# Performance work log

Hardware: AMD Instinct MI355X
Metric: run time of the kernel (lower is better)

The kernel has to match this reference:

```python
import jax, jax.numpy as jnp
import numpy as np

B, S, E = 4, 2048, 512
H, D = 8, 64  # n_head, attn_dim


def setup_inputs() -> dict:
    key = jax.random.key(0)
    ks = jax.random.split(key, 12)
    scale = 0.02
    return {
        "input_q": jax.random.normal(ks[0], (B, S, E), dtype=jnp.float32),
        "input_k": jax.random.normal(ks[1], (B, S, E), dtype=jnp.float32),
        "input_v": jax.random.normal(ks[2], (B, S, E), dtype=jnp.float32),
        "mask": jax.random.randint(ks[3], (B, S, S), 0, 2, dtype=jnp.int32),
        "wq": jax.random.normal(ks[4], (E, H * D), dtype=jnp.float32) * scale,
        "bq": jnp.zeros((H * D,), dtype=jnp.float32),
        "wk": jax.random.normal(ks[5], (E, H * D), dtype=jnp.float32) * scale,
        "bk": jnp.zeros((H * D,), dtype=jnp.float32),
        "wv": jax.random.normal(ks[6], (E, H * D), dtype=jnp.float32) * scale,
        "bv": jnp.zeros((H * D,), dtype=jnp.float32),
        "wo": jax.random.normal(ks[7], (H * D, E), dtype=jnp.float32) * scale,
        "bo": jnp.zeros((E,), dtype=jnp.float32),
    }


def reference(input_q, input_k, input_v, mask, wq, bq, wk, bk, wv, bv, wo, bo):
    b, lq, _ = input_q.shape
    lk = input_k.shape[1]
    # projections -> [b, len, H, D] -> [b, H, len, D]
    q = (input_q @ wq + bq).reshape(b, lq, H, D).transpose(0, 2, 1, 3)
    k = (input_k @ wk + bk).reshape(b, lk, H, D).transpose(0, 2, 1, 3)
    v = (input_v @ wv + bv).reshape(b, lk, H, D).transpose(0, 2, 1, 3)
    # raw scores [b, H, lq, lk]
    score = jnp.einsum("bhqd,bhkd->bhqk", q, k)
    # NOTE: original masks with -1e9 BEFORE dividing by sqrt(attn_dim)
    score = jnp.where(mask[:, None, :, :] == 0, jnp.float32(-1e9), score)
    attn = jax.nn.softmax(score / jnp.sqrt(jnp.float32(D)), axis=-1)
    out = jnp.einsum("bhqk,bhkd->bqhd", attn, v).reshape(b, lq, H * D)
    return out @ wo + bo
```

## Files before the change

### kernel.cpp

```cpp
#include <hip/hip_runtime.h>
#include <hip/hip_bf16.h>
#include <hip/hip_fp16.h>
#include <stdint.h>

#define Bc 4
#define Sc 2048
#define Ec 512
#define Hc 8
#define Dc 64
#define HDc 512

typedef __attribute__((ext_vector_type(8))) short bf16x8;
typedef __attribute__((ext_vector_type(4))) _Float16 f16x4;
typedef __attribute__((ext_vector_type(4))) float f32x4;
typedef unsigned int u32;

__device__ __forceinline__ unsigned short f2bf(float x) {
    union { float f; unsigned u; } v; v.f = x;
    unsigned r = v.u + 0x7FFFu + ((v.u >> 16) & 1u);
    return (unsigned short)(r >> 16);
}

__device__ __forceinline__ unsigned pkbf2(float a, float b) {
    float2 f; f.x = a; f.y = b;
    __hip_bfloat162 h = __float22bfloat162_rn(f);
    union { __hip_bfloat162 h2; unsigned u; } u; u.h2 = h;
    return u.u;
}

__device__ __forceinline__ unsigned short f2h(float x) {
    return __half_as_ushort(__float2half_rn(x));
}

__device__ __forceinline__ unsigned pkh2(float a, float b) {
    union { __half2 h2; unsigned u; } u;
    u.h2 = __floats2half2_rn(a, b);
    return u.u;
}

__device__ __forceinline__ uint4 pack8(float4 a, float4 b) {
    uint4 v;
    v.x = pkbf2(a.x, a.y); v.y = pkbf2(a.z, a.w);
    v.z = pkbf2(b.x, b.y); v.w = pkbf2(b.z, b.w);
    return v;
}

__device__ __forceinline__ void gload_lds(const void* g, void* l) {
    __builtin_amdgcn_global_load_lds(
        (const __attribute__((address_space(1))) u32*)g,
        (__attribute__((address_space(3))) u32*)l,
        16, 0, 0);
}

__global__ __launch_bounds__(256) void prep(
    const int* __restrict__ mask, unsigned long long* __restrict__ bits,
    const float* __restrict__ W0, const float* __restrict__ W1,
    const float* __restrict__ W2, const float* __restrict__ W3,
    unsigned short* __restrict__ Wt)
{
    const int blk = blockIdx.x;
    __shared__ float t[64][65];
    if (blk < 256) {
        const int z = blk >> 6;
        const float* W = z == 0 ? W0 : (z == 1 ? W1 : (z == 2 ? W2 : W3));
        unsigned short* O = Wt + (size_t)z * Ec * HDc;
        const int k0 = ((blk >> 3) & 7) * 64, n0 = (blk & 7) * 64;
#pragma unroll
        for (int i = 0; i < 16; i++) {
            int idx = threadIdx.x + 256 * i;
            int kr = idx >> 6, nc = idx & 63;
            t[nc][kr] = W[(size_t)(k0 + kr) * HDc + n0 + nc];
        }
        __syncthreads();
#pragma unroll
        for (int i = 0; i < 16; i++) {
            int idx = threadIdx.x + 256 * i;
            int nr = idx >> 6, kc = idx & 63;
            O[(size_t)(n0 + nr) * Ec + k0 + kc] = f2bf(t[nr][kc]);
        }
    } else {
        const int lane = threadIdx.x & 63;
        int wave = ((blk - 256) * 256 + (int)threadIdx.x) >> 6;
        const int nwaves = (2048 * 256) >> 6;
        const int nwords = (Bc * Sc * Sc) / 64;
        for (int w = wave; w < nwords; w += nwaves) {
            int m = mask[(size_t)w * 64 + lane];
            unsigned long long b = __ballot(m != 0);
            if (lane == 0) bits[w] = b;
        }
    }
}

__global__ __launch_bounds__(256) void proj_gemm(
    const float* __restrict__ Xq, const float* __restrict__ Xk, const float* __restrict__ Xv,
    const unsigned short* __restrict__ Wt,
    const float* __restrict__ bq, const float* __restrict__ bk, const float* __restrict__ bv,
    unsigned short* __restrict__ Oq, unsigned short* __restrict__ Ok,
    unsigned short* __restrict__ Vt)
{
    const int z = blockIdx.z;
    const float* X = z == 0 ? Xq : (z == 1 ? Xk : Xv);
    const unsigned short* Bt = Wt + (size_t)z * Ec * HDc;
    const float* bias = z == 0 ? bq : (z == 1 ? bk : bv);

    const int n0 = blockIdx.x * 128;
    const int m0 = blockIdx.y * 128;
    const int tid = threadIdx.x, lane = tid & 63, w = tid >> 6;
    const int c = lane & 15, quad = lane >> 4;
    const int wm = w & 1, wn = w >> 1;

    __shared__ unsigned short As[128 * 64];
    __shared__ unsigned short Bs[128 * 64];

    f32x4 acc[4][4];
#pragma unroll
    for (int i = 0; i < 4; i++)
#pragma unroll
        for (int j = 0; j < 4; j++) acc[i][j] = (f32x4){0.f, 0.f, 0.f, 0.f};

    for (int k0 = 0; k0 < Ec; k0 += 64) {
        __syncthreads();
#pragma unroll
        for (int jj = 0; jj < 4; jj++) {
            int rb = w * 32 + jj * 8;
            int row = rb + (lane >> 3);
            int dg = (lane & 7) ^ (row & 7);
            gload_lds(Bt + (size_t)(n0 + row) * Ec + k0 + dg * 8, &Bs[rb * 64]);
        }
#pragma unroll
        for (int s = 0; s < 4; s++) {
            int idx = tid + 256 * s;
            int row = idx >> 3, kp = idx & 7;
            int dg = kp ^ (row & 7);
            const float* src = X + (size_t)(m0 + row) * Ec + k0 + dg * 8;
            float4 fa = *(const float4*)src;
            float4 fb = *(const float4*)(src + 4);
            *(uint4*)&As[row * 64 + kp * 8] = pack8(fa, fb);
        }
        __syncthreads();
#pragma unroll
        for (int ks = 0; ks < 2; ks++) {
            int kg = ks * 4 + quad;
            bf16x8 af[4], bfr[4];
#pragma unroll
            for (int mt = 0; mt < 4; mt++) {
                int row = wm * 64 + mt * 16 + c;
                af[mt] = *(const bf16x8*)&As[row * 64 + ((kg ^ (row & 7)) * 8)];
            }
#pragma unroll
            for (int nt = 0; nt < 4; nt++) {
                int row = wn * 64 + nt * 16 + c;
                bfr[nt] = *(const bf16x8*)&Bs[row * 64 + ((kg ^ (row & 7)) * 8)];
            }
            if (z < 2) {
#pragma unroll
                for (int mt = 0; mt < 4; mt++)
#pragma unroll
                    for (int nt = 0; nt < 4; nt++)
                        acc[mt][nt] = __builtin_amdgcn_mfma_f32_16x16x32_bf16(af[mt], bfr[nt], acc[mt][nt], 0, 0, 0);
            } else {
#pragma unroll
                for (int mt = 0; mt < 4; mt++)
#pragma unroll
                    for (int nt = 0; nt < 4; nt++)
                        acc[mt][nt] = __builtin_amdgcn_mfma_f32_16x16x32_bf16(bfr[nt], af[mt], acc[mt][nt], 0, 0, 0);
            }
        }
    }

    if (z < 2) {
        unsigned short* O = z == 0 ? Oq : Ok;
        const float qs = z == 0 ? 0.125f : 1.0f;
#pragma unroll
        for (int mt = 0; mt < 4; mt++)
#pragma unroll
            for (int r = 0; r < 4; r++) {
                int gm = m0 + wm * 64 + mt * 16 + quad * 4 + r;
#pragma unroll
                for (int nt = 0; nt < 4; nt++) {
                    int gn = n0 + wn * 64 + nt * 16 + c;
                    O[(size_t)gm * HDc + gn] = f2bf((acc[mt][nt][r] + bias[gn]) * qs);
                }
            }
    } else {
#pragma unroll
        for (int mt = 0; mt < 4; mt++) {
            int gm = m0 + wm * 64 + mt * 16 + c;
            int bb = gm >> 11, sPos = gm & (Sc - 1);
#pragma unroll
            for (int nt = 0; nt < 4; nt++)
#pragma unroll
                for (int r = 0; r < 4; r++) {
                    int ng = n0 + wn * 64 + nt * 16 + quad * 4 + r;
                    int hh = ng >> 6, d = ng & 63;
                    Vt[((size_t)(bb * Hc + hh) * Dc + d) * Sc + sPos] = f2h(acc[mt][nt][r] + bias[ng]);
                }
        }
    }
}

__global__ __launch_bounds__(256, 4) void attn_kernel(
    const unsigned short* __restrict__ Qb, const unsigned short* __restrict__ Kb,
    const unsigned short* __restrict__ Vt, const unsigned long long* __restrict__ Mb,
    unsigned short* __restrict__ Ob)
{
    const int qt = blockIdx.x;
    const int h  = blockIdx.y;
    const int b  = blockIdx.z;
    const int q0 = qt * 64;
    const int tid = threadIdx.x, lane = tid & 63, w = tid >> 6;
    const int c = lane & 15, quad = lane >> 4;

    __shared__ unsigned short Ks[2][64 * 64];
    __shared__ unsigned short Vs[2][64 * 64];

    const int qg = q0 + w * 16 + c;
    const size_t qoff = ((size_t)b * Sc + qg) * HDc + h * Dc;

    bf16x8 qf[2];
    qf[0] = *(const bf16x8*)(Qb + qoff + quad * 8);
    qf[1] = *(const bf16x8*)(Qb + qoff + 32 + quad * 8);

    const unsigned long long* mr = Mb + ((size_t)b * Sc + qg) * (Sc / 64);
    const size_t kbase = ((size_t)b * Sc) * HDc + h * Dc;
    const size_t vbase = ((size_t)(b * Hc + h)) * Dc * Sc;

    f32x4 o[4], osum;
#pragma unroll
    for (int i = 0; i < 4; i++) o[i] = (f32x4){0.f, 0.f, 0.f, 0.f};
    osum = (f32x4){0.f, 0.f, 0.f, 0.f};

    const f16x4 ones = {(_Float16)1.0f, (_Float16)1.0f, (_Float16)1.0f, (_Float16)1.0f};

    auto stage = [&](int kt, int buf) {
#pragma unroll
        for (int j = 0; j < 2; j++) {
            int rb = w * 16 + j * 8;
            int row = rb + (lane >> 3);
            int dg = (lane & 7) ^ (row & 7);
            gload_lds(Kb + kbase + (size_t)(kt * 64 + row) * HDc + dg * 8, &Ks[buf][rb * 64]);
            gload_lds(Vt + vbase + (size_t)row * Sc + kt * 64 + dg * 8, &Vs[buf][rb * 64]);
        }
    };

    stage(0, 0);
    for (int kt = 0; kt < Sc / 64; kt++) {
        const int cur = kt & 1;
        unsigned long long mw = mr[kt];
        __syncthreads();
        if (kt + 1 < Sc / 64) stage(kt + 1, cur ^ 1);

        f32x4 s[4];
#pragma unroll
        for (int nt = 0; nt < 4; nt++) s[nt] = (f32x4){0.f, 0.f, 0.f, 0.f};
#pragma unroll
        for (int ks = 0; ks < 2; ks++) {
            int kg = ks * 4 + quad;
#pragma unroll
            for (int nt = 0; nt < 4; nt++) {
                int t = nt * 16 + c;
                bf16x8 a = *(const bf16x8*)&Ks[cur][t * 64 + ((kg ^ (t & 7)) * 8)];
                s[nt] = __builtin_amdgcn_mfma_f32_16x16x32_bf16(a, qf[ks], s[nt], 0, 0, 0);
            }
        }

        u32 mlo = (u32)(mw) >> (quad * 4);
        u32 mhi = (u32)(mw >> 32) >> (quad * 4);
        f16x4 pb[4];
#pragma unroll
        for (int nt = 0; nt < 4; nt++) {
            u32 msrc = (nt < 2) ? mlo : mhi;
            float p[4];
#pragma unroll
            for (int r = 0; r < 4; r++) {
                const int sh = (nt & 1) * 16 + r;
                int keep = ((int)(msrc << (31 - sh))) >> 31;
                float e = __expf(s[nt][r]);
                p[r] = __int_as_float(__float_as_int(e) & keep);
            }
            union { unsigned u[2]; f16x4 v; } pk;
            pk.u[0] = pkh2(p[0], p[1]);
            pk.u[1] = pkh2(p[2], p[3]);
            pb[nt] = pk.v;
        }

#pragma unroll
        for (int ntb = 0; ntb < 4; ntb++) {
#pragma unroll
            for (int dt = 0; dt < 4; dt++) {
                int d = dt * 16 + c;
                const f16x4 a = *(const f16x4*)&Vs[cur][d * 64 +
                    (((ntb * 2 + (quad >> 1)) ^ (d & 7)) * 8) + ((quad & 1) * 4)];
                o[dt] = __builtin_amdgcn_mfma_f32_16x16x16f16(a, pb[ntb], o[dt], 0, 0, 0);
            }
            osum = __builtin_amdgcn_mfma_f32_16x16x16f16(ones, pb[ntb], osum, 0, 0, 0);
        }
    }

    const float inv = 1.0f / osum[0];

#pragma unroll
    for (int nt = 0; nt < 4; nt++) {
        uint2 pk;
        pk.x = pkbf2(o[nt][0] * inv, o[nt][1] * inv);
        pk.y = pkbf2(o[nt][2] * inv, o[nt][3] * inv);
        *(uint2*)(Ob + qoff + nt * 16 + quad * 4) = pk;
    }
}

__global__ __launch_bounds__(256) void out_gemm(
    const unsigned short* __restrict__ Ab, const unsigned short* __restrict__ Bt,
    const float* __restrict__ bias, float* __restrict__ Out)
{
    const int n0 = blockIdx.x * 128;
    const int m0 = blockIdx.y * 64;
    const int tid = threadIdx.x, lane = tid & 63, w = tid >> 6;
    const int c = lane & 15, quad = lane >> 4;
    const int wm = w & 1, wn = w >> 1;

    __shared__ unsigned short As[64 * 64];
    __shared__ unsigned short Bs[128 * 64];

    f32x4 acc[2][4];
#pragma unroll
    for (int i = 0; i < 2; i++)
#pragma unroll
        for (int j = 0; j < 4; j++) acc[i][j] = (f32x4){0.f, 0.f, 0.f, 0.f};

    for (int k0 = 0; k0 < HDc; k0 += 64) {
        __syncthreads();
#pragma unroll
        for (int jj = 0; jj < 4; jj++) {
            int rb = w * 32 + jj * 8;
            int row = rb + (lane >> 3);
            int dg = (lane & 7) ^ (row & 7);
            gload_lds(Bt + (size_t)(n0 + row) * Ec + k0 + dg * 8, &Bs[rb * 64]);
        }
#pragma unroll
        for (int jj = 0; jj < 2; jj++) {
            int rb = w * 16 + jj * 8;
            int row = rb + (lane >> 3);
            int dg = (lane & 7) ^ (row & 7);
            gload_lds(Ab + (size_t)(m0 + row) * HDc + k0 + dg * 8, &As[rb * 64]);
        }
        __syncthreads();
#pragma unroll
        for (int ks = 0; ks < 2; ks++) {
            int kg = ks * 4 + quad;
            bf16x8 af[2], bfr[4];
#pragma unroll
            for (int mt = 0; mt < 2; mt++) {
                int row = wm * 32 + mt * 16 + c;
                af[mt] = *(const bf16x8*)&As[row * 64 + ((kg ^ (row & 7)) * 8)];
            }
#pragma unroll
            for (int nt = 0; nt < 4; nt++) {
                int row = wn * 64 + nt * 16 + c;
                bfr[nt] = *(const bf16x8*)&Bs[row * 64 + ((kg ^ (row & 7)) * 8)];
            }
#pragma unroll
            for (int mt = 0; mt < 2; mt++)
#pragma unroll
                for (int nt = 0; nt < 4; nt++)
                    acc[mt][nt] = __builtin_amdgcn_mfma_f32_16x16x32_bf16(af[mt], bfr[nt], acc[mt][nt], 0, 0, 0);
        }
    }
#pragma unroll
    for (int mt = 0; mt < 2; mt++)
#pragma unroll
        for (int r = 0; r < 4; r++) {
            int gm = m0 + wm * 32 + mt * 16 + quad * 4 + r;
#pragma unroll
            for (int nt = 0; nt < 4; nt++) {
                int gn = n0 + wn * 64 + nt * 16 + c;
                Out[(size_t)gm * Ec + gn] = acc[mt][nt][r] + bias[gn];
            }
        }
}

extern "C" void kernel_launch(void* const* d_in, const int* in_sizes, int n_in,
                              void* d_out, int out_size, void* d_ws, size_t ws_size,
                              hipStream_t stream)
{
    const float* xq = (const float*)d_in[0];
    const float* xk = (const float*)d_in[1];
    const float* xv = (const float*)d_in[2];
    const int* mask = (const int*)d_in[3];
    const float* wq = (const float*)d_in[4];
    const float* bq = (const float*)d_in[5];
    const float* wk = (const float*)d_in[6];
    const float* bk = (const float*)d_in[7];
    const float* wv = (const float*)d_in[8];
    const float* bv = (const float*)d_in[9];
    const float* wo = (const float*)d_in[10];
    const float* bo = (const float*)d_in[11];
    float* out = (float*)d_out;

    char* ws = (char*)d_ws;
    unsigned short* qb = (unsigned short*)(ws + (size_t)0 * 1024 * 1024);
    unsigned short* kb = (unsigned short*)(ws + (size_t)8 * 1024 * 1024);
    unsigned short* vt = (unsigned short*)(ws + (size_t)16 * 1024 * 1024);
    unsigned short* ab = (unsigned short*)(ws + (size_t)24 * 1024 * 1024);
    unsigned long long* mb = (unsigned long long*)(ws + (size_t)32 * 1024 * 1024);
    unsigned short* wt = (unsigned short*)(ws + (size_t)48 * 1024 * 1024);

    hipLaunchKernelGGL(prep, dim3(2304), dim3(256), 0, stream,
                       mask, mb, wq, wk, wv, wo, wt);

    const size_t WSZ = (size_t)Ec * HDc;
    hipLaunchKernelGGL(proj_gemm, dim3(4, 64, 3), dim3(256), 0, stream,
                       xq, xk, xv, wt, bq, bk, bv, qb, kb, vt);

    hipLaunchKernelGGL(attn_kernel, dim3(32, 8, 4), dim3(256), 0, stream,
                       qb, kb, vt, mb, ab);

    hipLaunchKernelGGL(out_gemm, dim3(4, 128), dim3(256), 0, stream,
                       ab, wt + 3 * WSZ, bo, out);
}
```

Baseline: 287.7 us.

## Pre-convert inputs to bf16, permute V layout, double query rows per attention wave

The prep kernel now also converts the fp32 Q/K/V inputs to bf16, so proj_gemm can stage A tiles with direct global-to-LDS loads instead of converting in registers. The V-transpose store uses a permuted sequence order so the attention kernel can read 8 fp16 values per LDS load. The attention kernel runs 128 threads per block with each wave handling 32 query rows, so every K/V fragment feeds two MFMA chains. The cost is a larger prep kernel with an extra bf16 round-trip through memory, plus more registers per wave in attention.

```diff
diff --git a/kernel.cpp b/kernel.cpp
--- a/kernel.cpp
+++ b/kernel.cpp
@@ -12,6 +12,7 @@
 
 typedef __attribute__((ext_vector_type(8))) short bf16x8;
 typedef __attribute__((ext_vector_type(4))) _Float16 f16x4;
+typedef __attribute__((ext_vector_type(8))) _Float16 f16x8;
 typedef __attribute__((ext_vector_type(4))) float f32x4;
 typedef unsigned int u32;
 
@@ -52,11 +53,17 @@
         16, 0, 0);
 }
 
+__device__ __forceinline__ int vperm(int mt, int c) {
+    return ((c >> 2) << 4) + ((mt >> 1) << 3) + ((mt & 1) << 2) + (c & 3);
+}
+
 __global__ __launch_bounds__(256) void prep(
     const int* __restrict__ mask, unsigned long long* __restrict__ bits,
     const float* __restrict__ W0, const float* __restrict__ W1,
     const float* __restrict__ W2, const float* __restrict__ W3,
-    unsigned short* __restrict__ Wt)
+    unsigned short* __restrict__ Wt,
+    const float* __restrict__ Xq, const float* __restrict__ Xk,
+    const float* __restrict__ Xv, unsigned short* __restrict__ Xb)
 {
     const int blk = blockIdx.x;
     __shared__ float t[64][65];
@@ -78,7 +85,7 @@
             int nr = idx >> 6, kc = idx & 63;
             O[(size_t)(n0 + nr) * Ec + k0 + kc] = f2bf(t[nr][kc]);
         }
-    } else {
+    } else if (blk < 2304) {
         const int lane = threadIdx.x & 63;
         int wave = ((blk - 256) * 256 + (int)threadIdx.x) >> 6;
         const int nwaves = (2048 * 256) >> 6;
@@ -88,18 +95,25 @@
             unsigned long long b = __ballot(m != 0);
             if (lane == 0) bits[w] = b;
         }
+    } else {
+        const int zi = blk - 2304;
+        const int z = zi >> 11, wi = zi & 2047;
+        const float* X = z == 0 ? Xq : (z == 1 ? Xk : Xv);
+        const size_t off = ((size_t)wi * 256 + threadIdx.x) * 8;
+        const float4* p = (const float4*)(X + off);
+        float4 f0 = p[0], f1 = p[1];
+        *(uint4*)(Xb + (size_t)z * 4194304 + off) = pack8(f0, f1);
     }
 }
 
 __global__ __launch_bounds__(256) void proj_gemm(
-    const float* __restrict__ Xq, const float* __restrict__ Xk, const float* __restrict__ Xv,
-    const unsigned short* __restrict__ Wt,
+    const unsigned short* __restrict__ Xb, const unsigned short* __restrict__ Wt,
     const float* __restrict__ bq, const float* __restrict__ bk, const float* __restrict__ bv,
     unsigned short* __restrict__ Oq, unsigned short* __restrict__ Ok,
     unsigned short* __restrict__ Vt)
 {
     const int z = blockIdx.z;
-    const float* X = z == 0 ? Xq : (z == 1 ? Xk : Xv);
+    const unsigned short* Xz = Xb + (size_t)z * 4194304;
     const unsigned short* Bt = Wt + (size_t)z * Ec * HDc;
     const float* bias = z == 0 ? bq : (z == 1 ? bk : bv);
 
@@ -126,16 +140,7 @@
             int row = rb + (lane >> 3);
             int dg = (lane & 7) ^ (row & 7);
             gload_lds(Bt + (size_t)(n0 + row) * Ec + k0 + dg * 8, &Bs[rb * 64]);
-        }
-#pragma unroll
-        for (int s = 0; s < 4; s++) {
-            int idx = tid + 256 * s;
-            int row = idx >> 3, kp = idx & 7;
-            int dg = kp ^ (row & 7);
-            const float* src = X + (size_t)(m0 + row) * Ec + k0 + dg * 8;
-            float4 fa = *(const float4*)src;
-            float4 fb = *(const float4*)(src + 4);
-            *(uint4*)&As[row * 64 + kp * 8] = pack8(fa, fb);
+            gload_lds(Xz + (size_t)(m0 + row) * Ec + k0 + dg * 8, &As[rb * 64]);
         }
         __syncthreads();
 #pragma unroll
@@ -187,19 +192,20 @@
         for (int mt = 0; mt < 4; mt++) {
             int gm = m0 + wm * 64 + mt * 16 + c;
             int bb = gm >> 11, sPos = gm & (Sc - 1);
+            int tbase = (sPos & ~63) + vperm(mt, c);
 #pragma unroll
             for (int nt = 0; nt < 4; nt++)
 #pragma unroll
                 for (int r = 0; r < 4; r++) {
                     int ng = n0 + wn * 64 + nt * 16 + quad * 4 + r;
                     int hh = ng >> 6, d = ng & 63;
-                    Vt[((size_t)(bb * Hc + hh) * Dc + d) * Sc + sPos] = f2h(acc[mt][nt][r] + bias[ng]);
+                    Vt[((size_t)(bb * Hc + hh) * Dc + d) * Sc + tbase] = f2h(acc[mt][nt][r] + bias[ng]);
                 }
         }
     }
 }
 
-__global__ __launch_bounds__(256, 4) void attn_kernel(
+__global__ __launch_bounds__(128, 2) void attn_kernel(
     const unsigned short* __restrict__ Qb, const unsigned short* __restrict__ Kb,
     const unsigned short* __restrict__ Vt, const unsigned long long* __restrict__ Mb,
     unsigned short* __restrict__ Ob)
@@ -214,28 +220,35 @@
     __shared__ unsigned short Ks[2][64 * 64];
     __shared__ unsigned short Vs[2][64 * 64];
 
-    const int qg = q0 + w * 16 + c;
-    const size_t qoff = ((size_t)b * Sc + qg) * HDc + h * Dc;
-
-    bf16x8 qf[2];
-    qf[0] = *(const bf16x8*)(Qb + qoff + quad * 8);
-    qf[1] = *(const bf16x8*)(Qb + qoff + 32 + quad * 8);
-
-    const unsigned long long* mr = Mb + ((size_t)b * Sc + qg) * (Sc / 64);
+    const int q_g0 = q0 + w * 32 + c;
+    const int q_g1 = q_g0 + 16;
+    const size_t qoff0 = ((size_t)b * Sc + q_g0) * HDc + h * Dc;
+    const size_t qoff1 = ((size_t)b * Sc + q_g1) * HDc + h * Dc;
+
+    bf16x8 qf0[2], qf1[2];
+#pragma unroll
+    for (int ks = 0; ks < 2; ks++) {
+        qf0[ks] = *(const bf16x8*)(Qb + qoff0 + ks * 32 + quad * 8);
+        qf1[ks] = *(const bf16x8*)(Qb + qoff1 + ks * 32 + quad * 8);
+    }
+
+    const unsigned long long* mr0 = Mb + ((size_t)b * Sc + q_g0) * (Sc / 64);
+    const unsigned long long* mr1 = Mb + ((size_t)b * Sc + q_g1) * (Sc / 64);
     const size_t kbase = ((size_t)b * Sc) * HDc + h * Dc;
     const size_t vbase = ((size_t)(b * Hc + h)) * Dc * Sc;
 
-    f32x4 o[4], osum;
-#pragma unroll
-    for (int i = 0; i < 4; i++) o[i] = (f32x4){0.f, 0.f, 0.f, 0.f};
-    osum = (f32x4){0.f, 0.f, 0.f, 0.f};
+    f32x4 o0[4], o1[4], osum0, osum1;
+#pragma unroll
+    for (int i = 0; i < 4; i++) { o0[i] = (f32x4){0.f,0.f,0.f,0.f}; o1[i] = (f32x4){0.f,0.f,0.f,0.f}; }
+    osum0 = (f32x4){0.f, 0.f, 0.f, 0.f};
+    osum1 = (f32x4){0.f, 0.f, 0.f, 0.f};
 
     const f16x4 ones = {(_Float16)1.0f, (_Float16)1.0f, (_Float16)1.0f, (_Float16)1.0f};
 
     auto stage = [&](int kt, int buf) {
 #pragma unroll
-        for (int j = 0; j < 2; j++) {
-            int rb = w * 16 + j * 8;
+        for (int j = 0; j < 4; j++) {
+            int rb = w * 32 + j * 8;
             int row = rb + (lane >> 3);
             int dg = (lane & 7) ^ (row & 7);
             gload_lds(Kb + kbase + (size_t)(kt * 64 + row) * HDc + dg * 8, &Ks[buf][rb * 64]);
@@ -246,13 +259,14 @@
     stage(0, 0);
     for (int kt = 0; kt < Sc / 64; kt++) {
         const int cur = kt & 1;
-        unsigned long long mw = mr[kt];
+        unsigned long long mw0 = mr0[kt];
+        unsigned long long mw1 = mr1[kt];
         __syncthreads();
         if (kt + 1 < Sc / 64) stage(kt + 1, cur ^ 1);
 
-        f32x4 s[4];
-#pragma unroll
-        for (int nt = 0; nt < 4; nt++) s[nt] = (f32x4){0.f, 0.f, 0.f, 0.f};
+        f32x4 s0[4], s1[4];
+#pragma unroll
+        for (int nt = 0; nt < 4; nt++) { s0[nt] = (f32x4){0.f,0.f,0.f,0.f}; s1[nt] = (f32x4){0.f,0.f,0.f,0.f}; }
 #pragma unroll
         for (int ks = 0; ks < 2; ks++) {
             int kg = ks * 4 + quad;
@@ -260,51 +274,65 @@
             for (int nt = 0; nt < 4; nt++) {
                 int t = nt * 16 + c;
                 bf16x8 a = *(const bf16x8*)&Ks[cur][t * 64 + ((kg ^ (t & 7)) * 8)];
-                s[nt] = __builtin_amdgcn_mfma_f32_16x16x32_bf16(a, qf[ks], s[nt], 0, 0, 0);
-            }
-        }
-
-        u32 mlo = (u32)(mw) >> (quad * 4);
-        u32 mhi = (u32)(mw >> 32) >> (quad * 4);
-        f16x4 pb[4];
+                s0[nt] = __builtin_amdgcn_mfma_f32_16x16x32_bf16(a, qf0[ks], s0[nt], 0, 0, 0);
+                s1[nt] = __builtin_amdgcn_mfma_f32_16x16x32_bf16(a, qf1[ks], s1[nt], 0, 0, 0);
+            }
+        }
+
+        u32 mlo0 = (u32)(mw0) >> (quad * 4), mhi0 = (u32)(mw0 >> 32) >> (quad * 4);
+        u32 mlo1 = (u32)(mw1) >> (quad * 4), mhi1 = (u32)(mw1 >> 32) >> (quad * 4);
+        f16x4 pb0[4], pb1[4];
 #pragma unroll
         for (int nt = 0; nt < 4; nt++) {
-            u32 msrc = (nt < 2) ? mlo : mhi;
-            float p[4];
+            u32 ms0 = (nt < 2) ? mlo0 : mhi0;
+            u32 ms1 = (nt < 2) ? mlo1 : mhi1;
+            float p0[4], p1[4];
 #pragma unroll
             for (int r = 0; r < 4; r++) {
                 const int sh = (nt & 1) * 16 + r;
-                int keep = ((int)(msrc << (31 - sh))) >> 31;
-                float e = __expf(s[nt][r]);
-                p[r] = __int_as_float(__float_as_int(e) & keep);
+                int k0 = ((int)(ms0 << (31 - sh))) >> 31;
+                int k1 = ((int)(ms1 << (31 - sh))) >> 31;
+                p0[r] = __int_as_float(__float_as_int(__expf(s0[nt][r])) & k0);
+                p1[r] = __int_as_float(__float_as_int(__expf(s1[nt][r])) & k1);
             }
             union { unsigned u[2]; f16x4 v; } pk;
-            pk.u[0] = pkh2(p[0], p[1]);
-            pk.u[1] = pkh2(p[2], p[3]);
-            pb[nt] = pk.v;
-        }
-
-#pragma unroll
-        for (int ntb = 0; ntb < 4; ntb++) {
+            pk.u[0] = pkh2(p0[0], p0[1]); pk.u[1] = pkh2(p0[2], p0[3]);
+            pb0[nt] = pk.v;
+            pk.u[0] = pkh2(p1[0], p1[1]); pk.u[1] = pkh2(p1[2], p1[3]);
+            pb1[nt] = pk.v;
+        }
+
+#pragma unroll
+        for (int a = 0; a < 2; a++) {
 #pragma unroll
             for (int dt = 0; dt < 4; dt++) {
                 int d = dt * 16 + c;
-                const f16x4 a = *(const f16x4*)&Vs[cur][d * 64 +
-                    (((ntb * 2 + (quad >> 1)) ^ (d & 7)) * 8) + ((quad & 1) * 4)];
-                o[dt] = __builtin_amdgcn_mfma_f32_16x16x16f16(a, pb[ntb], o[dt], 0, 0, 0);
-            }
-            osum = __builtin_amdgcn_mfma_f32_16x16x16f16(ones, pb[ntb], osum, 0, 0, 0);
-        }
-    }
-
-    const float inv = 1.0f / osum[0];
-
-#pragma unroll
-    for (int nt = 0; nt < 4; nt++) {
+                union { f16x8 v8; f16x4 v4[2]; } vv;
+                vv.v8 = *(const f16x8*)&Vs[cur][d * 64 + (((quad * 2 + a) ^ (d & 7)) * 8)];
+                o0[dt] = __builtin_amdgcn_mfma_f32_16x16x16f16(vv.v4[0], pb0[2*a],   o0[dt], 0, 0, 0);
+                o0[dt] = __builtin_amdgcn_mfma_f32_16x16x16f16(vv.v4[1], pb0[2*a+1], o0[dt], 0, 0, 0);
+                o1[dt] = __builtin_amdgcn_mfma_f32_16x16x16f16(vv.v4[0], pb1[2*a],   o1[dt], 0, 0, 0);
+                o1[dt] = __builtin_amdgcn_mfma_f32_16x16x16f16(vv.v4[1], pb1[2*a+1], o1[dt], 0, 0, 0);
+            }
+            osum0 = __builtin_amdgcn_mfma_f32_16x16x16f16(ones, pb0[2*a],   osum0, 0, 0, 0);
+            osum0 = __builtin_amdgcn_mfma_f32_16x16x16f16(ones, pb0[2*a+1], osum0, 0, 0, 0);
+            osum1 = __builtin_amdgcn_mfma_f32_16x16x16f16(ones, pb1[2*a],   osum1, 0, 0, 0);
+            osum1 = __builtin_amdgcn_mfma_f32_16x16x16f16(ones, pb1[2*a+1], osum1, 0, 0, 0);
+        }
+    }
+
+    const float inv0 = 1.0f / osum0[0];
+    const float inv1 = 1.0f / osum1[0];
+
+#pragma unroll
+    for (int dt = 0; dt < 4; dt++) {
         uint2 pk;
-        pk.x = pkbf2(o[nt][0] * inv, o[nt][1] * inv);
-        pk.y = pkbf2(o[nt][2] * inv, o[nt][3] * inv);
-        *(uint2*)(Ob + qoff + nt * 16 + quad * 4) = pk;
+        pk.x = pkbf2(o0[dt][0] * inv0, o0[dt][1] * inv0);
+        pk.y = pkbf2(o0[dt][2] * inv0, o0[dt][3] * inv0);
+        *(uint2*)(Ob + qoff0 + dt * 16 + quad * 4) = pk;
+        pk.x = pkbf2(o1[dt][0] * inv1, o1[dt][1] * inv1);
+        pk.y = pkbf2(o1[dt][2] * inv1, o1[dt][3] * inv1);
+        *(uint2*)(Ob + qoff1 + dt * 16 + quad * 4) = pk;
     }
 }
 
@@ -397,23 +425,24 @@
     float* out = (float*)d_out;
 
     char* ws = (char*)d_ws;
-    unsigned short* qb = (unsigned short*)(ws + (size_t)0 * 1024 * 1024);
-    unsigned short* kb = (unsigned short*)(ws + (size_t)8 * 1024 * 1024);
-    unsigned short* vt = (unsigned short*)(ws + (size_t)16 * 1024 * 1024);
-    unsigned short* ab = (unsigned short*)(ws + (size_t)24 * 1024 * 1024);
-    unsigned long long* mb = (unsigned long long*)(ws + (size_t)32 * 1024 * 1024);
-    unsigned short* wt = (unsigned short*)(ws + (size_t)48 * 1024 * 1024);
-
-    hipLaunchKernelGGL(prep, dim3(2304), dim3(256), 0, stream,
-                       mask, mb, wq, wk, wv, wo, wt);
-
-    const size_t WSZ = (size_t)Ec * HDc;
+    const size_t MB = 1024 * 1024;
+    unsigned short* qb = (unsigned short*)(ws + 0 * MB);
+    unsigned short* kb = (unsigned short*)(ws + 8 * MB);
+    unsigned short* vt = (unsigned short*)(ws + 16 * MB);
+    unsigned short* xb = (unsigned short*)(ws + 24 * MB);
+    unsigned short* ab = (unsigned short*)(ws + 24 * MB);
+    unsigned long long* mb = (unsigned long long*)(ws + 48 * MB);
+    unsigned short* wt = (unsigned short*)(ws + 50 * MB);
+
+    hipLaunchKernelGGL(prep, dim3(8448), dim3(256), 0, stream,
+                       mask, mb, wq, wk, wv, wo, wt, xq, xk, xv, xb);
+
     hipLaunchKernelGGL(proj_gemm, dim3(4, 64, 3), dim3(256), 0, stream,
-                       xq, xk, xv, wt, bq, bk, bv, qb, kb, vt);
-
-    hipLaunchKernelGGL(attn_kernel, dim3(32, 8, 4), dim3(256), 0, stream,
+                       xb, wt, bq, bk, bv, qb, kb, vt);
+
+    hipLaunchKernelGGL(attn_kernel, dim3(32, 8, 4), dim3(128), 0, stream,
                        qb, kb, vt, mb, ab);
 
     hipLaunchKernelGGL(out_gemm, dim3(4, 128), dim3(256), 0, stream,
-                       ab, wt + 3 * WSZ, bo, out);
-}
+                       ab, wt + 3 * (size_t)Ec * HDc, bo, out);
+}
```

Measured after the change: 292.2 us. Within noise of the previous version (+1.6%).
